# Kernel tuning notes

Hardware: AMD Instinct MI355X
Metric: run time of the kernel (lower is better)

The kernel has to match this reference:

```python
import jax, jax.numpy as jnp
import numpy as np

N = 400_000   # active voxels
C = 128       # inplanes = outplanes
K = 9         # nplanes*3*3 kernel offsets (nplanes=1)
EPS = 1e-4    # scn BatchNormalization default eps


def setup_inputs() -> dict:
    key = jax.random.key(0)
    ks = jax.random.split(key, 5)
    feat = jax.random.normal(ks[0], (N, C), dtype=jnp.float32)
    # rulebook: neighbor active-site index per kernel offset, plus validity mask
    nbr_idx = jax.random.randint(ks[1], (N, K), 0, N, dtype=jnp.int32)
    nbr_idx = nbr_idx.at[:, K // 2].set(jnp.arange(N, dtype=jnp.int32))  # center = self
    nbr_mask = jax.random.uniform(ks[2], (N, K)) < 0.6
    nbr_mask = nbr_mask.at[:, K // 2].set(True)
    scale = 1.0 / np.sqrt(K * C)
    W1 = jax.random.normal(ks[3], (K, C, C), dtype=jnp.float32) * scale
    W2 = jax.random.normal(ks[4], (K, C, C), dtype=jnp.float32) * scale
    gamma1 = jnp.ones((C,), jnp.float32)
    beta1 = jnp.zeros((C,), jnp.float32)
    gamma2 = jnp.ones((C,), jnp.float32)
    beta2 = jnp.zeros((C,), jnp.float32)
    return {"feat": feat, "W1": W1, "W2": W2,
            "gamma1": gamma1, "beta1": beta1,
            "gamma2": gamma2, "beta2": beta2,
            "nbr_idx": nbr_idx, "nbr_mask": nbr_mask}


def _subm_conv(feat, nbr_idx, nbr_mask, W):
    # rulebook gather -> GEMM -> accumulate; output lives at the same active sites
    out = jnp.zeros((feat.shape[0], W.shape[2]), feat.dtype)
    for k in range(W.shape[0]):  # small fixed K=9 structural loop
        xk = jnp.where(nbr_mask[:, k:k + 1], feat[nbr_idx[:, k]], 0.0)
        out = out + xk @ W[k]
    return out


def _batchnorm(x, gamma, beta):
    mu = jnp.mean(x, axis=0)
    var = jnp.mean(jnp.square(x - mu), axis=0)
    return (x - mu) * (gamma * jax.lax.rsqrt(var + EPS)) + beta


def reference(feat, W1, W2, gamma1, beta1, gamma2, beta2, nbr_idx, nbr_mask):
    residual = feat                                   # scn.Identity (stride=1)
    out = _subm_conv(feat, nbr_idx, nbr_mask, W1)     # conv1
    out = jax.nn.relu(_batchnorm(out, gamma1, beta1))  # BatchNormReLU
    out = _subm_conv(out, nbr_idx, nbr_mask, W2)      # conv2
    out = _batchnorm(out, gamma2, beta2)              # bn2
    return jax.nn.relu(out + residual)                # AddTable + ReLU
```

## Files before the change

kernel.cpp:

```cpp
#include <hip/hip_runtime.h>


#define C_CH 128
#define K_OFF 9
#define MTILE 64

typedef __attribute__((ext_vector_type(8))) short bf16x8;
typedef __attribute__((ext_vector_type(4))) float f32x4;
typedef __attribute__((ext_vector_type(8))) unsigned short u16x8;

typedef __attribute__((address_space(1))) const unsigned int* gas_p;
typedef __attribute__((address_space(3))) unsigned int* las_p;

__device__ __forceinline__ void gload_lds16(const unsigned short* g, unsigned short* l) {
    __builtin_amdgcn_global_load_lds((gas_p)g, (las_p)l, 16, 0, 0);
}

__device__ __forceinline__ unsigned short f2b(float f) {
    union { float f; unsigned u; } v; v.f = f;
    unsigned r = v.u + 0x7fffu + ((v.u >> 16) & 1u);
    return (unsigned short)(r >> 16);
}
__device__ __forceinline__ float b2f(unsigned short h) {
    union { unsigned u; float f; } v; v.u = ((unsigned)h) << 16;
    return v.f;
}


__global__ void init_detect_k(float* stats, unsigned int* zrow1, unsigned int* zrow2,
                              const unsigned char* __restrict__ m, int* flagA, int* flagB) {
    int t = threadIdx.x;
    if (blockIdx.x == 0) {
        if (t < 256) { stats[t] = 0.f; stats[256 + t] = 0.f; }
        if (t >= 256 && t < 258) ((int*)stats)[1024 + (t - 256)] = 0;
        if (t < 64) { zrow1[t] = 0u; zrow2[t] = 0u; }
    } else {
        int i = (blockIdx.x - 1) * 256 + t;
        unsigned char v = m[i];
        if ((i & 3) != 0 && v != 0) atomicOr(flagA, 1);
        if (v > 1) atomicOr(flagB, 1);
    }
}

__global__ void prep_k(const float* __restrict__ x, unsigned short* __restrict__ y, int n4,
                       const float* __restrict__ W1, unsigned short* __restrict__ Wp1,
                       const float* __restrict__ W2, unsigned short* __restrict__ Wp2,
                       const int* __restrict__ nidx, const void* __restrict__ m,
                       const int* __restrict__ flagA, const int* __restrict__ flagB,
                       int* __restrict__ eidx, int NK, int N) {
    const int PACK = K_OFF * 8 * 4 * 512;
    int fa = *flagA, fb = *flagB;
    int i = blockIdx.x * blockDim.x + threadIdx.x;
    int s = gridDim.x * blockDim.x;
    int tot = n4 + 2 * PACK + NK;
    for (; i < tot; i += s) {
        if (i < n4) {
            float4 f = ((const float4*)x)[i];
            ushort4 o;
            o.x = f2b(f.x); o.y = f2b(f.y); o.z = f2b(f.z); o.w = f2b(f.w);
            ((ushort4*)y)[i] = o;
        } else if (i < n4 + 2 * PACK) {
            int ii = i - n4;
            const float* W = (ii < PACK) ? W1 : W2;
            unsigned short* Wp = (ii < PACK) ? Wp1 : Wp2;
            if (ii >= PACK) ii -= PACK;
            int j = ii & 7;
            int l = (ii >> 3) & 63;
            int frag = ii >> 9;
            int ks = frag & 3;
            int nt = (frag >> 2) & 7;
            int ko = frag >> 5;
            int cin = ks * 32 + (l >> 4) * 8 + j;
            int cout = nt * 16 + (l & 15);
            Wp[ii] = f2b(W[ko * C_CH * C_CH + cin * C_CH + cout]);
        } else {
            int j = i - n4 - 2 * PACK;
            bool t;
            if (!fa)       t = ((const int*)m)[j] != 0;
            else if (fb)   t = ((const unsigned*)m)[j] != 0;
            else           t = ((const unsigned char*)m)[j] != 0;
            eidx[j] = t ? nidx[j] : N;
        }
    }
}


__global__ __launch_bounds__(256, 3) void conv_kernel(
    const unsigned short* __restrict__ Xb,
    const unsigned short* __restrict__ Wp,
    const int* __restrict__ eidx,
    unsigned short* __restrict__ Yraw,
    float* __restrict__ statS, float* __restrict__ statQ)
{
    const int tid = threadIdx.x;
    const int lane = tid & 63;
    const int wv = tid >> 6;
    const int tile = blockIdx.x * MTILE;
    const int asub = lane >> 4;
    const int l15 = lane & 15;

    __shared__ alignas(16) unsigned short At[3][MTILE * C_CH];
    __shared__ int sIdxT[K_OFF][MTILE];

    for (int i = tid; i < MTILE * K_OFF; i += 256) {
        int r = i / K_OFF, k = i - r * K_OFF;
        sIdxT[k][r] = eidx[(size_t)(tile + r) * K_OFF + k];
    }
    __syncthreads();

    const int r_st = tid >> 4;
    const int ch_st = tid & 15;

    #define STAGE(buf, ko)                                                        \
        {                                                                         \
            _Pragma("unroll")                                                     \
            for (int jr = 0; jr < 4; ++jr) {                                      \
                int r = jr * 16 + r_st;                                           \
                int g = sIdxT[ko][r];                                             \
                const unsigned short* src =                                       \
                    Xb + (size_t)g * C_CH + ((ch_st ^ (r & 7)) * 8);              \
                unsigned short* dst = &At[buf][r * C_CH + ch_st * 8];             \
                gload_lds16(src, dst);                                            \
            }                                                                     \
        }

    #define LOADB0(ko)                                                            \
        {                                                                         \
            const unsigned short* wb = Wp + (size_t)(ko) * (8 * 4 * 512) + lane * 8; \
            _Pragma("unroll")                                                     \
            for (int ks = 0; ks < 4; ++ks) {                                      \
                b0a[ks] = *(const bf16x8*)(wb + ((wv * 2 + 0) * 4 + ks) * 512);   \
                b0b[ks] = *(const bf16x8*)(wb + ((wv * 2 + 1) * 4 + ks) * 512);   \
            }                                                                     \
        }
    #define LOADB1(ko)                                                            \
        {                                                                         \
            const unsigned short* wb = Wp + (size_t)(ko) * (8 * 4 * 512) + lane * 8; \
            _Pragma("unroll")                                                     \
            for (int ks = 0; ks < 4; ++ks) {                                      \
                b1a[ks] = *(const bf16x8*)(wb + ((wv * 2 + 0) * 4 + ks) * 512);   \
                b1b[ks] = *(const bf16x8*)(wb + ((wv * 2 + 1) * 4 + ks) * 512);   \
            }                                                                     \
        }

    f32x4 acc[4][2];
    #pragma unroll
    for (int m = 0; m < 4; ++m) { acc[m][0] = (f32x4){0,0,0,0}; acc[m][1] = (f32x4){0,0,0,0}; }

    bf16x8 b0a[4], b0b[4], b1a[4], b1b[4];

    STAGE(0, 0);
    LOADB0(0);
    STAGE(1, 1);

    #define CONV_ITER(KO, BA, BB, LB, VM)                                         \
        {                                                                         \
            if ((KO) + 1 < K_OFF) { LB((KO) + 1); }                               \
            __builtin_amdgcn_sched_barrier(0);                                    \
            asm volatile("s_waitcnt vmcnt(" #VM ")" ::: "memory");                \
            __builtin_amdgcn_s_barrier();                                         \
            __builtin_amdgcn_sched_barrier(0);                                    \
            if ((KO) + 2 < K_OFF) { STAGE((((KO) + 2) % 3), (KO) + 2); }          \
            __builtin_amdgcn_s_setprio(1);                                        \
            _Pragma("unroll")                                                     \
            for (int m = 0; m < 4; ++m) {                                         \
                bf16x8 a[4];                                                      \
                _Pragma("unroll")                                                 \
                for (int ks = 0; ks < 4; ++ks) {                                  \
                    int row = m * 16 + l15;                                       \
                    int sc = (ks * 4 + asub) ^ (row & 7);                         \
                    a[ks] = *(const bf16x8*)((const char*)At[(KO) % 3] + row * 256 + sc * 16); \
                }                                                                 \
                _Pragma("unroll")                                                 \
                for (int ks = 0; ks < 4; ++ks) {                                  \
                    acc[m][0] = __builtin_amdgcn_mfma_f32_16x16x32_bf16(a[ks], BA[ks], acc[m][0], 0, 0, 0); \
                    acc[m][1] = __builtin_amdgcn_mfma_f32_16x16x32_bf16(a[ks], BB[ks], acc[m][1], 0, 0, 0); \
                }                                                                 \
            }                                                                     \
            __builtin_amdgcn_s_setprio(0);                                        \
        }

    CONV_ITER(0, b0a, b0b, LOADB1, 12)
    CONV_ITER(1, b1a, b1b, LOADB0, 12)
    CONV_ITER(2, b0a, b0b, LOADB1, 12)
    CONV_ITER(3, b1a, b1b, LOADB0, 12)
    CONV_ITER(4, b0a, b0b, LOADB1, 12)
    CONV_ITER(5, b1a, b1b, LOADB0, 12)
    CONV_ITER(6, b0a, b0b, LOADB1, 12)
    CONV_ITER(7, b1a, b1b, LOADB0, 12)
    CONV_ITER(8, b0a, b0b, LOADB1, 0)
    #undef CONV_ITER
    #undef STAGE
    #undef LOADB0
    #undef LOADB1

    #pragma unroll
    for (int j = 0; j < 2; ++j) {
        float s = 0.f, q = 0.f;
        #pragma unroll
        for (int m = 0; m < 4; ++m)
            #pragma unroll
            for (int r = 0; r < 4; ++r) { float v = acc[m][j][r]; s += v; q += v * v; }
        s += __shfl_xor(s, 16); s += __shfl_xor(s, 32);
        q += __shfl_xor(q, 16); q += __shfl_xor(q, 32);
        if (lane < 16) {
            atomicAdd(&statS[wv * 32 + j * 16 + lane], s);
            atomicAdd(&statQ[wv * 32 + j * 16 + lane], q);
        }
    }

    #pragma unroll
    for (int m = 0; m < 4; ++m)
        #pragma unroll
        for (int j = 0; j < 2; ++j) {
            int col = (wv * 2 + j) * 16 + l15;
            #pragma unroll
            for (int r = 0; r < 4; ++r) {
                int row = tile + m * 16 + asub * 4 + r;
                Yraw[(size_t)row * C_CH + col] = f2b(acc[m][j][r]);
            }
        }
}


__global__ void finalize_bn_k(const float* __restrict__ S, const float* __restrict__ Q,
                              const float* __restrict__ gamma, const float* __restrict__ beta,
                              float* __restrict__ scale, float* __restrict__ bias, float invN) {
    int c = threadIdx.x;
    if (c < C_CH) {
        float mu = S[c] * invN;
        float var = Q[c] * invN - mu * mu;
        float inv = rsqrtf(var + 1e-4f);
        float sc = gamma[c] * inv;
        scale[c] = sc;
        bias[c] = beta[c] - mu * sc;
    }
}

__global__ void bn_relu_k(unsigned short* __restrict__ y,
                          const float* __restrict__ scale, const float* __restrict__ bias, int n8) {
    int i0 = blockIdx.x * blockDim.x + threadIdx.x;
    int S = gridDim.x * blockDim.x;
    int c0 = (i0 * 8) & (C_CH - 1);
    float sc[8], bs[8];
    #pragma unroll
    for (int j = 0; j < 8; ++j) { sc[j] = scale[c0 + j]; bs[j] = bias[c0 + j]; }
    for (int i = i0; i < n8; i += S) {
        u16x8 v = ((const u16x8*)y)[i];
        #pragma unroll
        for (int j = 0; j < 8; ++j) {
            float x = b2f((unsigned short)v[j]);
            x = fmaxf(x * sc[j] + bs[j], 0.f);
            v[j] = (short)f2b(x);
        }
        ((u16x8*)y)[i] = v;
    }
}

__global__ void final_fuse_k(const unsigned short* __restrict__ raw,
                             const float* __restrict__ feat,
                             const float* __restrict__ scale, const float* __restrict__ bias,
                             float* __restrict__ out, int n4) {
    int i0 = blockIdx.x * blockDim.x + threadIdx.x;
    int S = gridDim.x * blockDim.x;
    int c0 = (i0 * 4) & (C_CH - 1);
    float sc[4], bs[4];
    #pragma unroll
    for (int j = 0; j < 4; ++j) { sc[j] = scale[c0 + j]; bs[j] = bias[c0 + j]; }
    for (int i = i0; i < n4; i += S) {
        ushort4 r = ((const ushort4*)raw)[i];
        float4 f = ((const float4*)feat)[i];
        float4 o;
        o.x = fmaxf(b2f(r.x) * sc[0] + bs[0] + f.x, 0.f);
        o.y = fmaxf(b2f(r.y) * sc[1] + bs[1] + f.y, 0.f);
        o.z = fmaxf(b2f(r.z) * sc[2] + bs[2] + f.z, 0.f);
        o.w = fmaxf(b2f(r.w) * sc[3] + bs[3] + f.w, 0.f);
        ((float4*)out)[i] = o;
    }
}


extern "C" void kernel_launch(void* const* d_in, const int* in_sizes, int n_in,
                              void* d_out, int out_size, void* d_ws, size_t ws_size,
                              hipStream_t stream) {
    const float* feat = (const float*)d_in[0];
    const float* W1 = (const float*)d_in[1];
    const float* W2 = (const float*)d_in[2];
    const float* g1 = (const float*)d_in[3];
    const float* b1 = (const float*)d_in[4];
    const float* g2 = (const float*)d_in[5];
    const float* b2 = (const float*)d_in[6];
    const int* nidx = (const int*)d_in[7];
    const void* nmask = d_in[8];

    const int N = in_sizes[0] / C_CH;
    const int NK = N * K_OFF;

    char* ws = (char*)d_ws;
    unsigned short* featb = (unsigned short*)ws;
    size_t off = (size_t)(N + 1) * C_CH * 2;
    off = (off + 255) & ~(size_t)255;
    unsigned short* Wp1 = (unsigned short*)(ws + off); off += (size_t)K_OFF * C_CH * C_CH * 2;
    unsigned short* Wp2 = (unsigned short*)(ws + off); off += (size_t)K_OFF * C_CH * C_CH * 2;
    float* stats = (float*)(ws + off);
    float* S1 = stats;        float* Q1 = stats + 128;
    float* S2 = stats + 256;  float* Q2 = stats + 384;
    float* sc1 = stats + 512; float* bi1 = stats + 640;
    float* sc2 = stats + 768; float* bi2 = stats + 896;
    int* flagA = ((int*)stats) + 1024;
    int* flagB = ((int*)stats) + 1025;

    unsigned short* y1 = (unsigned short*)d_out;
    int* eidx = (int*)((char*)d_out + (size_t)134217728);
    unsigned short* out2raw = featb;

    hipLaunchKernelGGL(init_detect_k, dim3(65), dim3(256), 0, stream,
                       stats, (unsigned int*)(featb + (size_t)N * C_CH),
                       (unsigned int*)(y1 + (size_t)N * C_CH),
                       (const unsigned char*)nmask, flagA, flagB);
    hipLaunchKernelGGL(prep_k, dim3(2048), dim3(256), 0, stream,
                       feat, featb, N * C_CH / 4,
                       W1, Wp1, W2, Wp2,
                       nidx, nmask, flagA, flagB, eidx, NK, N);

    hipLaunchKernelGGL(conv_kernel, dim3(N / MTILE), dim3(256), 0, stream,
                       featb, Wp1, eidx, y1, S1, Q1);
    hipLaunchKernelGGL(finalize_bn_k, dim3(1), dim3(128), 0, stream, S1, Q1, g1, b1, sc1, bi1, 1.0f / N);
    hipLaunchKernelGGL(bn_relu_k, dim3(2048), dim3(256), 0, stream, y1, sc1, bi1, N * C_CH / 8);

    hipLaunchKernelGGL(conv_kernel, dim3(N / MTILE), dim3(256), 0, stream,
                       y1, Wp2, eidx, out2raw, S2, Q2);
    hipLaunchKernelGGL(finalize_bn_k, dim3(1), dim3(128), 0, stream, S2, Q2, g2, b2, sc2, bi2, 1.0f / N);
    hipLaunchKernelGGL(final_fuse_k, dim3(2048), dim3(256), 0, stream,
                       out2raw, feat, sc2, bi2, (float*)d_out, N * C_CH / 4);
}
```

Baseline: 565.5 us.

## Split conv K-loop into half-channel phases with smaller LDS stages

Each kernel offset is now staged as two 64-channel halves, so the triple LDS buffer holds half-row tiles (24KB instead of 48KB), with a new XOR swizzle for the 64-byte rows. The loop runs 18 finer-grained phases with adjusted vmcnt waits, and launch bounds rise from 3 to 5 blocks per CU. The aim is higher occupancy and finer gather/MFMA overlap to hide the random-gather latency. The cost is twice as many barriers per tile and possible register pressure under the tighter launch bound.

```diff
diff --git a/kernel.cpp b/kernel.cpp
--- a/kernel.cpp
+++ b/kernel.cpp
@@ -85,7 +85,7 @@
 }
 
 
-__global__ __launch_bounds__(256, 3) void conv_kernel(
+__global__ __launch_bounds__(256, 5) void conv_kernel(
     const unsigned short* __restrict__ Xb,
     const unsigned short* __restrict__ Wp,
     const int* __restrict__ eidx,
@@ -99,7 +99,7 @@
     const int asub = lane >> 4;
     const int l15 = lane & 15;
 
-    __shared__ alignas(16) unsigned short At[3][MTILE * C_CH];
+    __shared__ alignas(16) unsigned short At[3 * 4096];
     __shared__ int sIdxT[K_OFF][MTILE];
 
     for (int i = tid; i < MTILE * K_OFF; i += 256) {
@@ -108,20 +108,18 @@
     }
     __syncthreads();
 
-    const int r_st = tid >> 4;
-    const int ch_st = tid & 15;
-
-    #define STAGE(buf, ko)                                                        \
+    const int r_st = tid >> 2;
+    const int c_st = tid & 3;
+    const int sx_st = c_st ^ ((r_st >> 1) & 3);
+
+    #define STAGE(buf, P)                                                         \
         {                                                                         \
-            _Pragma("unroll")                                                     \
-            for (int jr = 0; jr < 4; ++jr) {                                      \
-                int r = jr * 16 + r_st;                                           \
-                int g = sIdxT[ko][r];                                             \
-                const unsigned short* src =                                       \
-                    Xb + (size_t)g * C_CH + ((ch_st ^ (r & 7)) * 8);              \
-                unsigned short* dst = &At[buf][r * C_CH + ch_st * 8];             \
-                gload_lds16(src, dst);                                            \
-            }                                                                     \
+            int g_ = sIdxT[(P) >> 1][r_st];                                       \
+            const unsigned short* rowp = Xb + (size_t)g_ * C_CH + ((P) & 1) * 64; \
+            gload_lds16(rowp + (0 * 4 + sx_st) * 8,                               \
+                        &At[(buf) * 4096 + 0 * 2048 + r_st * 32 + c_st * 8]);     \
+            gload_lds16(rowp + (1 * 4 + sx_st) * 8,                               \
+                        &At[(buf) * 4096 + 1 * 2048 + r_st * 32 + c_st * 8]);     \
         }
 
     #define LOADB0(ko)                                                            \
@@ -150,46 +148,52 @@
     bf16x8 b0a[4], b0b[4], b1a[4], b1b[4];
 
     STAGE(0, 0);
+    STAGE(1, 1);
     LOADB0(0);
-    STAGE(1, 1);
-
-    #define CONV_ITER(KO, BA, BB, LB, VM)                                         \
+
+    #define PHASE(P, H, VM, BA, BB, LBSTMT)                                       \
         {                                                                         \
-            if ((KO) + 1 < K_OFF) { LB((KO) + 1); }                               \
+            LBSTMT;                                                               \
             __builtin_amdgcn_sched_barrier(0);                                    \
             asm volatile("s_waitcnt vmcnt(" #VM ")" ::: "memory");                \
             __builtin_amdgcn_s_barrier();                                         \
             __builtin_amdgcn_sched_barrier(0);                                    \
-            if ((KO) + 2 < K_OFF) { STAGE((((KO) + 2) % 3), (KO) + 2); }          \
+            if ((P) + 2 < 18) { STAGE(((P) + 2) % 3, (P) + 2); }                  \
             __builtin_amdgcn_s_setprio(1);                                        \
             _Pragma("unroll")                                                     \
             for (int m = 0; m < 4; ++m) {                                         \
-                bf16x8 a[4];                                                      \
-                _Pragma("unroll")                                                 \
-                for (int ks = 0; ks < 4; ++ks) {                                  \
-                    int row = m * 16 + l15;                                       \
-                    int sc = (ks * 4 + asub) ^ (row & 7);                         \
-                    a[ks] = *(const bf16x8*)((const char*)At[(KO) % 3] + row * 256 + sc * 16); \
-                }                                                                 \
-                _Pragma("unroll")                                                 \
-                for (int ks = 0; ks < 4; ++ks) {                                  \
-                    acc[m][0] = __builtin_amdgcn_mfma_f32_16x16x32_bf16(a[ks], BA[ks], acc[m][0], 0, 0, 0); \
-                    acc[m][1] = __builtin_amdgcn_mfma_f32_16x16x32_bf16(a[ks], BB[ks], acc[m][1], 0, 0, 0); \
-                }                                                                 \
+                int R = m * 16 + l15;                                             \
+                const char* ab = (const char*)At + ((P) % 3) * 8192 + R * 64      \
+                                 + ((asub ^ ((R >> 1) & 3)) * 16);                \
+                bf16x8 a0 = *(const bf16x8*)(ab);                                 \
+                bf16x8 a1 = *(const bf16x8*)(ab + 4096);                          \
+                acc[m][0] = __builtin_amdgcn_mfma_f32_16x16x32_bf16(a0, BA[(H) * 2 + 0], acc[m][0], 0, 0, 0); \
+                acc[m][1] = __builtin_amdgcn_mfma_f32_16x16x32_bf16(a0, BB[(H) * 2 + 0], acc[m][1], 0, 0, 0); \
+                acc[m][0] = __builtin_amdgcn_mfma_f32_16x16x32_bf16(a1, BA[(H) * 2 + 1], acc[m][0], 0, 0, 0); \
+                acc[m][1] = __builtin_amdgcn_mfma_f32_16x16x32_bf16(a1, BB[(H) * 2 + 1], acc[m][1], 0, 0, 0); \
             }                                                                     \
             __builtin_amdgcn_s_setprio(0);                                        \
         }
 
-    CONV_ITER(0, b0a, b0b, LOADB1, 12)
-    CONV_ITER(1, b1a, b1b, LOADB0, 12)
-    CONV_ITER(2, b0a, b0b, LOADB1, 12)
-    CONV_ITER(3, b1a, b1b, LOADB0, 12)
-    CONV_ITER(4, b0a, b0b, LOADB1, 12)
-    CONV_ITER(5, b1a, b1b, LOADB0, 12)
-    CONV_ITER(6, b0a, b0b, LOADB1, 12)
-    CONV_ITER(7, b1a, b1b, LOADB0, 12)
-    CONV_ITER(8, b0a, b0b, LOADB1, 0)
-    #undef CONV_ITER
+    PHASE(0,  0, 8,  b0a, b0b, LOADB1(1))
+    PHASE(1,  1, 10, b0a, b0b, {})
+    PHASE(2,  0, 10, b1a, b1b, LOADB0(2))
+    PHASE(3,  1, 10, b1a, b1b, {})
+    PHASE(4,  0, 10, b0a, b0b, LOADB1(3))
+    PHASE(5,  1, 10, b0a, b0b, {})
+    PHASE(6,  0, 10, b1a, b1b, LOADB0(4))
+    PHASE(7,  1, 10, b1a, b1b, {})
+    PHASE(8,  0, 10, b0a, b0b, LOADB1(5))
+    PHASE(9,  1, 10, b0a, b0b, {})
+    PHASE(10, 0, 10, b1a, b1b, LOADB0(6))
+    PHASE(11, 1, 10, b1a, b1b, {})
+    PHASE(12, 0, 10, b0a, b0b, LOADB1(7))
+    PHASE(13, 1, 10, b0a, b0b, {})
+    PHASE(14, 0, 10, b1a, b1b, LOADB0(8))
+    PHASE(15, 1, 10, b1a, b1b, {})
+    PHASE(16, 0, 2,  b0a, b0b, {})
+    PHASE(17, 1, 0,  b0a, b0b, {})
+    #undef PHASE
     #undef STAGE
     #undef LOADB0
     #undef LOADB1
```

After: 846.8 us. +49.7%, slower.

## Fuse rulebook mask into conv kernel and double-buffer gathers for higher occupancy

Applied to the files above, without the earlier changes.

Drops the separate eidx pass from prep_k. Each conv block now reads the mask and neighbour indices directly and builds its index table in LDS. The A-tile staging goes from a triple buffer (prefetch two ahead) to a double buffer (prefetch one ahead), which cuts LDS use so launch bounds can rise to 4 blocks per CU, and the vmcnt waits are adjusted to match. The trade is a shallower prefetch that may expose more gather latency, plus the mask decode being done twice (once per conv) in exchange for removing a full-size eidx write and read.

```diff
diff --git a/kernel.cpp b/kernel.cpp
--- a/kernel.cpp
+++ b/kernel.cpp
@@ -44,22 +44,18 @@
 
 __global__ void prep_k(const float* __restrict__ x, unsigned short* __restrict__ y, int n4,
                        const float* __restrict__ W1, unsigned short* __restrict__ Wp1,
-                       const float* __restrict__ W2, unsigned short* __restrict__ Wp2,
-                       const int* __restrict__ nidx, const void* __restrict__ m,
-                       const int* __restrict__ flagA, const int* __restrict__ flagB,
-                       int* __restrict__ eidx, int NK, int N) {
+                       const float* __restrict__ W2, unsigned short* __restrict__ Wp2) {
     const int PACK = K_OFF * 8 * 4 * 512;
-    int fa = *flagA, fb = *flagB;
     int i = blockIdx.x * blockDim.x + threadIdx.x;
     int s = gridDim.x * blockDim.x;
-    int tot = n4 + 2 * PACK + NK;
+    int tot = n4 + 2 * PACK;
     for (; i < tot; i += s) {
         if (i < n4) {
             float4 f = ((const float4*)x)[i];
             ushort4 o;
             o.x = f2b(f.x); o.y = f2b(f.y); o.z = f2b(f.z); o.w = f2b(f.w);
             ((ushort4*)y)[i] = o;
-        } else if (i < n4 + 2 * PACK) {
+        } else {
             int ii = i - n4;
             const float* W = (ii < PACK) ? W1 : W2;
             unsigned short* Wp = (ii < PACK) ? Wp1 : Wp2;
@@ -73,22 +69,18 @@
             int cin = ks * 32 + (l >> 4) * 8 + j;
             int cout = nt * 16 + (l & 15);
             Wp[ii] = f2b(W[ko * C_CH * C_CH + cin * C_CH + cout]);
-        } else {
-            int j = i - n4 - 2 * PACK;
-            bool t;
-            if (!fa)       t = ((const int*)m)[j] != 0;
-            else if (fb)   t = ((const unsigned*)m)[j] != 0;
-            else           t = ((const unsigned char*)m)[j] != 0;
-            eidx[j] = t ? nidx[j] : N;
-        }
-    }
-}
-
-
-__global__ __launch_bounds__(256, 3) void conv_kernel(
+        }
+    }
+}
+
+
+__global__ __launch_bounds__(256, 4) void conv_kernel(
     const unsigned short* __restrict__ Xb,
     const unsigned short* __restrict__ Wp,
-    const int* __restrict__ eidx,
+    const int* __restrict__ nidx,
+    const void* __restrict__ nmask,
+    const int* __restrict__ flagA, const int* __restrict__ flagB,
+    int Nzero,
     unsigned short* __restrict__ Yraw,
     float* __restrict__ statS, float* __restrict__ statQ)
 {
@@ -99,12 +91,20 @@
     const int asub = lane >> 4;
     const int l15 = lane & 15;
 
-    __shared__ alignas(16) unsigned short At[3][MTILE * C_CH];
+    __shared__ alignas(16) unsigned short At[2][MTILE * C_CH];
     __shared__ int sIdxT[K_OFF][MTILE];
 
-    for (int i = tid; i < MTILE * K_OFF; i += 256) {
-        int r = i / K_OFF, k = i - r * K_OFF;
-        sIdxT[k][r] = eidx[(size_t)(tile + r) * K_OFF + k];
+    {
+        int fa = *flagA, fb = *flagB;
+        for (int i = tid; i < MTILE * K_OFF; i += 256) {
+            int r = i / K_OFF, k = i - r * K_OFF;
+            size_t gi = (size_t)(tile + r) * K_OFF + k;
+            bool t;
+            if (!fa)       t = ((const int*)nmask)[gi] != 0;
+            else if (fb)   t = ((const unsigned*)nmask)[gi] != 0;
+            else           t = ((const unsigned char*)nmask)[gi] != 0;
+            sIdxT[k][r] = t ? nidx[gi] : Nzero;
+        }
     }
     __syncthreads();
 
@@ -151,7 +151,6 @@
 
     STAGE(0, 0);
     LOADB0(0);
-    STAGE(1, 1);
 
     #define CONV_ITER(KO, BA, BB, LB, VM)                                         \
         {                                                                         \
@@ -160,7 +159,7 @@
             asm volatile("s_waitcnt vmcnt(" #VM ")" ::: "memory");                \
             __builtin_amdgcn_s_barrier();                                         \
             __builtin_amdgcn_sched_barrier(0);                                    \
-            if ((KO) + 2 < K_OFF) { STAGE((((KO) + 2) % 3), (KO) + 2); }          \
+            if ((KO) + 1 < K_OFF) { STAGE(((KO) + 1) & 1, (KO) + 1); }            \
             __builtin_amdgcn_s_setprio(1);                                        \
             _Pragma("unroll")                                                     \
             for (int m = 0; m < 4; ++m) {                                         \
@@ -169,7 +168,7 @@
                 for (int ks = 0; ks < 4; ++ks) {                                  \
                     int row = m * 16 + l15;                                       \
                     int sc = (ks * 4 + asub) ^ (row & 7);                         \
-                    a[ks] = *(const bf16x8*)((const char*)At[(KO) % 3] + row * 256 + sc * 16); \
+                    a[ks] = *(const bf16x8*)((const char*)At[(KO) & 1] + row * 256 + sc * 16); \
                 }                                                                 \
                 _Pragma("unroll")                                                 \
                 for (int ks = 0; ks < 4; ++ks) {                                  \
@@ -180,14 +179,14 @@
             __builtin_amdgcn_s_setprio(0);                                        \
         }
 
-    CONV_ITER(0, b0a, b0b, LOADB1, 12)
-    CONV_ITER(1, b1a, b1b, LOADB0, 12)
-    CONV_ITER(2, b0a, b0b, LOADB1, 12)
-    CONV_ITER(3, b1a, b1b, LOADB0, 12)
-    CONV_ITER(4, b0a, b0b, LOADB1, 12)
-    CONV_ITER(5, b1a, b1b, LOADB0, 12)
-    CONV_ITER(6, b0a, b0b, LOADB1, 12)
-    CONV_ITER(7, b1a, b1b, LOADB0, 12)
+    CONV_ITER(0, b0a, b0b, LOADB1, 8)
+    CONV_ITER(1, b1a, b1b, LOADB0, 8)
+    CONV_ITER(2, b0a, b0b, LOADB1, 8)
+    CONV_ITER(3, b1a, b1b, LOADB0, 8)
+    CONV_ITER(4, b0a, b0b, LOADB1, 8)
+    CONV_ITER(5, b1a, b1b, LOADB0, 8)
+    CONV_ITER(6, b0a, b0b, LOADB1, 8)
+    CONV_ITER(7, b1a, b1b, LOADB0, 8)
     CONV_ITER(8, b0a, b0b, LOADB1, 0)
     #undef CONV_ITER
     #undef STAGE
@@ -294,7 +293,6 @@
     const void* nmask = d_in[8];
 
     const int N = in_sizes[0] / C_CH;
-    const int NK = N * K_OFF;
 
     char* ws = (char*)d_ws;
     unsigned short* featb = (unsigned short*)ws;
@@ -311,7 +309,6 @@
     int* flagB = ((int*)stats) + 1025;
 
     unsigned short* y1 = (unsigned short*)d_out;
-    int* eidx = (int*)((char*)d_out + (size_t)134217728);
     unsigned short* out2raw = featb;
 
     hipLaunchKernelGGL(init_detect_k, dim3(65), dim3(256), 0, stream,
@@ -320,16 +317,15 @@
                        (const unsigned char*)nmask, flagA, flagB);
     hipLaunchKernelGGL(prep_k, dim3(2048), dim3(256), 0, stream,
                        feat, featb, N * C_CH / 4,
-                       W1, Wp1, W2, Wp2,
-                       nidx, nmask, flagA, flagB, eidx, NK, N);
+                       W1, Wp1, W2, Wp2);
 
     hipLaunchKernelGGL(conv_kernel, dim3(N / MTILE), dim3(256), 0, stream,
-                       featb, Wp1, eidx, y1, S1, Q1);
+                       featb, Wp1, nidx, nmask, flagA, flagB, N, y1, S1, Q1);
     hipLaunchKernelGGL(finalize_bn_k, dim3(1), dim3(128), 0, stream, S1, Q1, g1, b1, sc1, bi1, 1.0f / N);
     hipLaunchKernelGGL(bn_relu_k, dim3(2048), dim3(256), 0, stream, y1, sc1, bi1, N * C_CH / 8);
 
     hipLaunchKernelGGL(conv_kernel, dim3(N / MTILE), dim3(256), 0, stream,
-                       y1, Wp2, eidx, out2raw, S2, Q2);
+                       y1, Wp2, nidx, nmask, flagA, flagB, N, out2raw, S2, Q2);
     hipLaunchKernelGGL(finalize_bn_k, dim3(1), dim3(128), 0, stream, S2, Q2, g2, b2, sc2, bi2, 1.0f / N);
     hipLaunchKernelGGL(final_fuse_k, dim3(2048), dim3(256), 0, stream,
                        out2raw, feat, sc2, bi2, (float*)d_out, N * C_CH / 4);
```

After: 618.9 us. 9.4% more time.
